# Performance work log

Measured on AMD Instinct MI355X. Metric: run time of the kernel, lower is better.

The kernel has to match this reference:

```python
import jax, jax.numpy as jnp
import numpy as np

MAXT = 10000
BATCH = 4096
LOG_GAMMA = float(np.log(1.02))
ALPHA = float(np.log(0.99) / 1000.0)
INIT_LOGW = float(np.log(0.248))
INIT_LOGP = float(np.log(0.001))
TEMPERATURE = 1000.0
EPS = 1e-12


def setup_inputs() -> dict:
    key = jax.random.key(0)
    k1, k2 = jax.random.split(key)
    # actions are initialized to -10 in the original module (must be << 0 so exp(a) < 1)
    acts = -10.0 * jnp.ones((MAXT,), dtype=jnp.float32)
    u1 = jax.random.uniform(k1, (MAXT, BATCH), dtype=jnp.float32)
    u2 = jax.random.uniform(k2, (MAXT, BATCH), dtype=jnp.float32)
    return {"acts": acts, "u1": u1, "u2": u2}


def _gumbel_sigmoid(logp, uu1, uu2):
    # logit = logp - log(1 - exp(logp))
    logit = logp - jnp.log1p(-jnp.exp(logp))
    noise = -jnp.log(jnp.log(uu2 + EPS) / jnp.log(uu1 + EPS) + EPS)
    soft = jax.nn.sigmoid(logit + noise)  # gumbel_temp = 1
    hard = (soft > 0.5).astype(soft.dtype)
    # straight-through: hard value, soft gradient
    return soft + jax.lax.stop_gradient(hard - soft)


def reference(acts, u1, u2):
    def step(carry, xs):
        logp, logw, alive, cumrew = carry
        a, uu1, uu2 = xs
        alive = alive * (1.0 - _gumbel_sigmoid(logp, uu1, uu2))
        f = jnp.exp(a)
        new_logw = logw + LOG_GAMMA + jnp.log(1.0 - f)
        new_logp = logp + ALPHA * f * jnp.exp(logw)
        rwd = alive * jnp.exp(new_logw / TEMPERATURE)
        return (new_logp, new_logw, alive, cumrew + rwd), None

    batch = u1.shape[1]
    init = (
        jnp.full((batch,), INIT_LOGP, dtype=jnp.float32),
        jnp.full((batch,), INIT_LOGW, dtype=jnp.float32),
        jnp.ones((batch,), dtype=jnp.float32),
        jnp.zeros((batch,), dtype=jnp.float32),
    )
    (_, _, _, cumrew), _ = jax.lax.scan(step, init, (acts, u1, u2))
    return cumrew.mean()
```

## Files before the change

### kernel.cpp

```cpp
#include <hip/hip_runtime.h>

#define MAXT 10000
#define BATCH 4096
#define NT_SETUP 512
#define SEG 20
#define TCHUNK 16
#define CUT_LOGIT -27.7f

__device__ __forceinline__ float block_exscan(float v, float* sh, int tid) {
    sh[tid] = v;
    __syncthreads();
    for (int off = 1; off < NT_SETUP; off <<= 1) {
        float x = (tid >= off) ? sh[tid - off] : 0.0f;
        __syncthreads();
        sh[tid] += x;
        __syncthreads();
    }
    float excl = (tid > 0) ? sh[tid - 1] : 0.0f;
    __syncthreads();
    return excl;
}

__global__ __launch_bounds__(NT_SETUP) void setup_kernel(
    const float* __restrict__ acts,
    float* __restrict__ logit,
    float* __restrict__ rpref,
    float* __restrict__ cbuf,
    int*   __restrict__ tcut,
    int*   __restrict__ firstfire)
{
    __shared__ float sh[NT_SETUP];
    __shared__ int   shi[NT_SETUP];
    const int tid = threadIdx.x;

    const float LOG_GAMMA = 1.9802627296e-2f;
    const float ALPHA     = -1.0050335854e-5f;
    const float INIT_LOGW = -1.3943265329f;
    const float INIT_LOGP = -6.9077552790f;

    for (int i = tid; i < BATCH; i += NT_SETUP) firstfire[i] = MAXT;

    const int t0 = tid * SEG;
    const int n  = (t0 < MAXT) ? min(SEG, MAXT - t0) : 0;

    float lsum = 0.0f;
    for (int i = 0; i < n; ++i) {
        float f = expf(acts[t0 + i]);
        lsum += LOG_GAMMA + logf(1.0f - f);
    }
    float excl = block_exscan(lsum, sh, tid);
    float run = INIT_LOGW + excl;
    for (int i = 0; i < n; ++i) {
        int t = t0 + i;
        float f = expf(acts[t]);
        float d = LOG_GAMMA + logf(1.0f - f);
        cbuf[t]  = ALPHA * f * expf(run);
        rpref[t] = expf((run + d) * (1.0f / 1000.0f));
        run += d;
    }

    float csum = 0.0f;
    for (int i = 0; i < n; ++i) csum += cbuf[t0 + i];
    excl = block_exscan(csum, sh, tid);
    float logp = INIT_LOGP + excl;
    int localFirst = MAXT;
    for (int i = 0; i < n; ++i) {
        int t = t0 + i;
        float lg = logp - log1pf(-expf(logp));
        logit[t] = lg;
        if (localFirst == MAXT && lg <= CUT_LOGIT) localFirst = t;
        logp += cbuf[t];
    }
    shi[tid] = localFirst;
    __syncthreads();
    for (int off = NT_SETUP / 2; off > 0; off >>= 1) {
        if (tid < off) shi[tid] = min(shi[tid], shi[tid + off]);
        __syncthreads();
    }
    if (tid == 0) tcut[0] = shi[0];

    float rsum = 0.0f;
    for (int i = 0; i < n; ++i) rsum += rpref[t0 + i];
    excl = block_exscan(rsum, sh, tid);
    float rrun = excl;
    for (int i = 0; i < n; ++i) {
        int t = t0 + i;
        float v = rpref[t];
        rpref[t] = rrun;
        rrun += v;
    }
    if (n > 0 && (t0 + n) == MAXT) rpref[MAXT] = rrun;
}

__global__ __launch_bounds__(256) void scan_kernel(
    const float* __restrict__ u1, const float* __restrict__ u2,
    const float* __restrict__ logit, const int* __restrict__ tcutp,
    int* __restrict__ firstfire)
{
    __shared__ int   s_tcut;
    __shared__ float s_logit[TCHUNK];
    const int tid = threadIdx.x;
    if (tid == 0) s_tcut = *tcutp;
    __syncthreads();
    const int tcut = s_tcut;
    const int tstart = blockIdx.y * TCHUNK;
    if (tstart >= tcut) return;
    const int tend = min(tstart + TCHUNK, tcut);
    if (tid < tend - tstart) s_logit[tid] = logit[tstart + tid];
    __syncthreads();

    const int b = blockIdx.x * 256 + tid;
    const float EPSF = 1e-12f;
    int found = MAXT;
    for (int t = tstart; t < tend; ++t) {
        float a = u1[(size_t)t * BATCH + b];
        float c = u2[(size_t)t * BATCH + b];
        float noise = -logf(logf(c + EPSF) / logf(a + EPSF) + EPSF);
        if (s_logit[t - tstart] + noise > 0.0f) { found = t; break; }
    }
    if (found != MAXT) atomicMin(firstfire + b, found);
}

__global__ __launch_bounds__(1024) void finalize_kernel(
    const int* __restrict__ firstfire, const float* __restrict__ rpref,
    float* __restrict__ out)
{
    __shared__ double ssum[1024];
    const int tid = threadIdx.x;
    double s = 0.0;
    for (int i = tid; i < BATCH; i += 1024) {
        int t = firstfire[i];
        s += (double)rpref[t];
    }
    ssum[tid] = s;
    __syncthreads();
    for (int off = 512; off > 0; off >>= 1) {
        if (tid < off) ssum[tid] += ssum[tid + off];
        __syncthreads();
    }
    if (tid == 0) out[0] = (float)(ssum[0] / (double)BATCH);
}

extern "C" void kernel_launch(void* const* d_in, const int* in_sizes, int n_in,
                              void* d_out, int out_size, void* d_ws, size_t ws_size,
                              hipStream_t stream) {
    const float* acts = (const float*)d_in[0];
    const float* u1   = (const float*)d_in[1];
    const float* u2   = (const float*)d_in[2];
    float* out = (float*)d_out;

    float* W       = (float*)d_ws;
    float* logit   = W;
    float* rpref   = W + MAXT;
    float* cbuf    = W + 2 * MAXT + 4;
    int*   tcut    = (int*)(W + 3 * MAXT + 8);
    int*   ffire   = tcut + 4;

    setup_kernel<<<1, NT_SETUP, 0, stream>>>(acts, logit, rpref, cbuf, tcut, ffire);

    dim3 grid(BATCH / 256, (MAXT + TCHUNK - 1) / TCHUNK);
    scan_kernel<<<grid, 256, 0, stream>>>(u1, u2, logit, tcut, ffire);

    finalize_kernel<<<1, 1024, 0, stream>>>(ffire, rpref, out);
}
```

Measured before the change: 317.5 us.

## Rewrite fire test as log comparison, vectorize loads, use persistent grid

The per-step Gumbel test is rewritten algebraically: the logit plus noise threshold becomes a comparison of log(u2) against exp(logit) times log(u1), with a gate value precomputed in setup. This removes the division and the outer log and uses fast __logf intrinsics. The scan kernel now processes four batch elements per thread with float4 loads and uses a fixed grid of 80 y-blocks that stride over time chunks, no longer launching one block per chunk. The early break per element is gone, so every time step up to the cutoff is read and evaluated, and the fast intrinsics and dropped epsilon terms may change rounding near the threshold.

```diff
diff --git a/kernel.cpp b/kernel.cpp
--- a/kernel.cpp
+++ b/kernel.cpp
@@ -5,6 +5,7 @@
 #define NT_SETUP 512
 #define SEG 20
 #define TCHUNK 16
+#define NYB 80
 #define CUT_LOGIT -27.7f
 
 __device__ __forceinline__ float block_exscan(float v, float* sh, int tid) {
@@ -23,7 +24,7 @@
 
 __global__ __launch_bounds__(NT_SETUP) void setup_kernel(
     const float* __restrict__ acts,
-    float* __restrict__ logit,
+    float* __restrict__ gate,
     float* __restrict__ rpref,
     float* __restrict__ cbuf,
     int*   __restrict__ tcut,
@@ -67,7 +68,7 @@
     for (int i = 0; i < n; ++i) {
         int t = t0 + i;
         float lg = logp - log1pf(-expf(logp));
-        logit[t] = lg;
+        gate[t] = expf(lg) - 1e-12f;
         if (localFirst == MAXT && lg <= CUT_LOGIT) localFirst = t;
         logp += cbuf[t];
     }
@@ -94,31 +95,45 @@
 
 __global__ __launch_bounds__(256) void scan_kernel(
     const float* __restrict__ u1, const float* __restrict__ u2,
-    const float* __restrict__ logit, const int* __restrict__ tcutp,
+    const float* __restrict__ gate, const int* __restrict__ tcutp,
     int* __restrict__ firstfire)
 {
-    __shared__ int   s_tcut;
-    __shared__ float s_logit[TCHUNK];
     const int tid = threadIdx.x;
-    if (tid == 0) s_tcut = *tcutp;
-    __syncthreads();
-    const int tcut = s_tcut;
-    const int tstart = blockIdx.y * TCHUNK;
-    if (tstart >= tcut) return;
-    const int tend = min(tstart + TCHUNK, tcut);
-    if (tid < tend - tstart) s_logit[tid] = logit[tstart + tid];
-    __syncthreads();
+    const int b4  = (blockIdx.x * 256 + tid) * 4;
+    const int tcut = *tcutp;
+    const float E = 1e-12f;
 
-    const int b = blockIdx.x * 256 + tid;
-    const float EPSF = 1e-12f;
-    int found = MAXT;
-    for (int t = tstart; t < tend; ++t) {
-        float a = u1[(size_t)t * BATCH + b];
-        float c = u2[(size_t)t * BATCH + b];
-        float noise = -logf(logf(c + EPSF) / logf(a + EPSF) + EPSF);
-        if (s_logit[t - tstart] + noise > 0.0f) { found = t; break; }
+    int f0 = MAXT, f1 = MAXT, f2 = MAXT, f3 = MAXT;
+
+    for (int chunk = blockIdx.y; chunk * TCHUNK < tcut; chunk += gridDim.y) {
+        const int tbase = chunk * TCHUNK;
+        #pragma unroll
+        for (int g = 0; g < TCHUNK / 4; ++g) {
+            float4 a[4], c[4];
+            float gv[4];
+            #pragma unroll
+            for (int j = 0; j < 4; ++j) {
+                const int t = tbase + g * 4 + j;
+                a[j]  = *(const float4*)(u1 + (size_t)t * BATCH + b4);
+                c[j]  = *(const float4*)(u2 + (size_t)t * BATCH + b4);
+                gv[j] = gate[t];
+            }
+            #pragma unroll
+            for (int j = 0; j < 4; ++j) {
+                const int t = tbase + g * 4 + j;
+                const float k = gv[j];
+                if (__logf(c[j].x + E) > k * __logf(a[j].x + E)) f0 = min(f0, t);
+                if (__logf(c[j].y + E) > k * __logf(a[j].y + E)) f1 = min(f1, t);
+                if (__logf(c[j].z + E) > k * __logf(a[j].z + E)) f2 = min(f2, t);
+                if (__logf(c[j].w + E) > k * __logf(a[j].w + E)) f3 = min(f3, t);
+            }
+        }
     }
-    if (found != MAXT) atomicMin(firstfire + b, found);
+
+    if (f0 != MAXT) atomicMin(firstfire + b4 + 0, f0);
+    if (f1 != MAXT) atomicMin(firstfire + b4 + 1, f1);
+    if (f2 != MAXT) atomicMin(firstfire + b4 + 2, f2);
+    if (f3 != MAXT) atomicMin(firstfire + b4 + 3, f3);
 }
 
 __global__ __launch_bounds__(1024) void finalize_kernel(
@@ -150,16 +165,16 @@
     float* out = (float*)d_out;
 
     float* W       = (float*)d_ws;
-    float* logit   = W;
+    float* gate    = W;
     float* rpref   = W + MAXT;
     float* cbuf    = W + 2 * MAXT + 4;
     int*   tcut    = (int*)(W + 3 * MAXT + 8);
     int*   ffire   = tcut + 4;
 
-    setup_kernel<<<1, NT_SETUP, 0, stream>>>(acts, logit, rpref, cbuf, tcut, ffire);
+    setup_kernel<<<1, NT_SETUP, 0, stream>>>(acts, gate, rpref, cbuf, tcut, ffire);
 
-    dim3 grid(BATCH / 256, (MAXT + TCHUNK - 1) / TCHUNK);
-    scan_kernel<<<grid, 256, 0, stream>>>(u1, u2, logit, tcut, ffire);
+    dim3 grid(BATCH / (256 * 4), NYB);
+    scan_kernel<<<grid, 256, 0, stream>>>(u1, u2, gate, tcut, ffire);
 
     finalize_kernel<<<1, 1024, 0, stream>>>(ffire, rpref, out);
 }
```

New measurement: 315.3 us. About the same (-0.7%).
